# Kernel optimization log

Measured on AMD Instinct MI355X. Metric: run time of the kernel, lower is better.

The kernel has to match this reference:

```python
import jax, jax.numpy as jnp
import numpy as np

TEMPERATURE = 0.1
TOP_K = 8


def setup_inputs() -> dict:
    key = jax.random.key(0)
    k1, k2, k3 = jax.random.split(key, 3)
    num_tokens, d_model, num_experts = 32768, 2048, 64
    x = jax.random.normal(k1, (num_tokens, d_model), dtype=jnp.float32)
    # nn.Linear default init: U(-1/sqrt(fan_in), 1/sqrt(fan_in))
    bound = 1.0 / np.sqrt(d_model)
    W = jax.random.uniform(k2, (num_experts, d_model), jnp.float32, -bound, bound)
    b = jax.random.uniform(k3, (num_experts,), jnp.float32, -bound, bound)
    return {"x": x, "W": W, "b": b}


def reference(x, W, b):
    # gate: [T, E] = x @ W^T + b, scaled by temperature
    routing_logits = (jnp.einsum('td,ed->te', x, W) + b) / TEMPERATURE
    routing_probs = jax.nn.softmax(routing_logits, axis=-1)
    top_k_probs, top_k_indices = jax.lax.top_k(routing_probs, TOP_K)
    top_k_probs_normalized = top_k_probs / jnp.sum(top_k_probs, axis=-1, keepdims=True)
    return routing_logits, top_k_probs_normalized, top_k_indices
```

## Files before the change

### kernel.cpp

```cpp
#include <hip/hip_runtime.h>
#include <cstdint>

#define T_TOKENS 32768
#define D_MODEL  2048
#define N_EXP    64
#define BM       64
#define BK       64
#define CHUNKS   (D_MODEL / BK)
#define LDK      (BK + 8)

typedef short bf16x8 __attribute__((ext_vector_type(8)));
typedef unsigned short u16x8 __attribute__((ext_vector_type(8)));
typedef float f32x4 __attribute__((ext_vector_type(4)));

__device__ __forceinline__ unsigned short f2bf(float f) {
    union { float f; unsigned int u; } c; c.f = f;
    unsigned int u = c.u;
    u += 0x7fffu + ((u >> 16) & 1u);
    return (unsigned short)(u >> 16);
}
__device__ __forceinline__ float bf2f(unsigned short h) {
    union { float f; unsigned int u; } c; c.u = ((unsigned int)h) << 16;
    return c.f;
}

__device__ __forceinline__ void split3(const float4& a, const float4& b,
                                       u16x8& h, u16x8& m, u16x8& l) {
    float f[8] = {a.x, a.y, a.z, a.w, b.x, b.y, b.z, b.w};
#pragma unroll
    for (int i = 0; i < 8; ++i) {
        unsigned short hh = f2bf(f[i]);
        float r1 = f[i] - bf2f(hh);
        unsigned short mm = f2bf(r1);
        float r2 = r1 - bf2f(mm);
        unsigned short ll = f2bf(r2);
        h[i] = hh; m[i] = mm; l[i] = ll;
    }
}

__global__ __launch_bounds__(256, 2) void router_gemm(
    const float* __restrict__ x, const float* __restrict__ W,
    const float* __restrict__ b, float* __restrict__ logits)
{
    __shared__ unsigned short Ah[BM * LDK], Amid[BM * LDK], Alo[BM * LDK];
    __shared__ unsigned short Bh[N_EXP * LDK], Bmid[N_EXP * LDK], Blo[N_EXP * LDK];

    const int tid = threadIdx.x;
    const int t0  = blockIdx.x * BM;
    const int kq  = tid & 7;
    const int rid = tid >> 3;

    const float* xg = x + (long)(t0 + rid) * D_MODEL + kq * 8;
    const float* wg = W + (long)rid * D_MODEL + kq * 8;

    const int lane = tid & 63;
    const int w    = tid >> 6;
    const int ln   = lane & 15;
    const int kq8  = (lane >> 4) * 8;
    const int aoff = (w * 16 + ln) * LDK;

    f32x4 accA[4], accB[4];
#pragma unroll
    for (int j = 0; j < 4; ++j) { accA[j] = (f32x4)(0.f); accB[j] = (f32x4)(0.f); }

    float4 xr[2][2], wr[2][2];
#pragma unroll
    for (int p = 0; p < 2; ++p) {
        xr[p][0] = *(const float4*)(xg + (long)p * 32 * D_MODEL);
        xr[p][1] = *(const float4*)(xg + (long)p * 32 * D_MODEL + 4);
        wr[p][0] = *(const float4*)(wg + (long)p * 32 * D_MODEL);
        wr[p][1] = *(const float4*)(wg + (long)p * 32 * D_MODEL + 4);
    }

    for (int c = 0; c < CHUNKS; ++c) {
#pragma unroll
        for (int p = 0; p < 2; ++p) {
            const int row = rid + p * 32;
            u16x8 h, m, l;
            split3(xr[p][0], xr[p][1], h, m, l);
            *(u16x8*)&Ah  [row * LDK + kq * 8] = h;
            *(u16x8*)&Amid[row * LDK + kq * 8] = m;
            *(u16x8*)&Alo [row * LDK + kq * 8] = l;
            split3(wr[p][0], wr[p][1], h, m, l);
            *(u16x8*)&Bh  [row * LDK + kq * 8] = h;
            *(u16x8*)&Bmid[row * LDK + kq * 8] = m;
            *(u16x8*)&Blo [row * LDK + kq * 8] = l;
        }
        if (c + 1 < CHUNKS) {
            const float* xn = xg + (c + 1) * BK;
            const float* wn = wg + (c + 1) * BK;
#pragma unroll
            for (int p = 0; p < 2; ++p) {
                xr[p][0] = *(const float4*)(xn + (long)p * 32 * D_MODEL);
                xr[p][1] = *(const float4*)(xn + (long)p * 32 * D_MODEL + 4);
                wr[p][0] = *(const float4*)(wn + (long)p * 32 * D_MODEL);
                wr[p][1] = *(const float4*)(wn + (long)p * 32 * D_MODEL + 4);
            }
        }
        __syncthreads();
#pragma unroll
        for (int ks = 0; ks < 2; ++ks) {
            const int ko = ks * 32 + kq8;
            bf16x8 ah = *(const bf16x8*)&Ah  [aoff + ko];
            bf16x8 am = *(const bf16x8*)&Amid[aoff + ko];
            bf16x8 al = *(const bf16x8*)&Alo [aoff + ko];
#pragma unroll
            for (int j = 0; j < 4; ++j) {
                const int boff = (j * 16 + ln) * LDK + ko;
                bf16x8 bh = *(const bf16x8*)&Bh  [boff];
                bf16x8 bm = *(const bf16x8*)&Bmid[boff];
                bf16x8 bl = *(const bf16x8*)&Blo [boff];
                accA[j] = __builtin_amdgcn_mfma_f32_16x16x32_bf16(ah, bh, accA[j], 0, 0, 0);
                accB[j] = __builtin_amdgcn_mfma_f32_16x16x32_bf16(am, bh, accB[j], 0, 0, 0);
                accB[j] = __builtin_amdgcn_mfma_f32_16x16x32_bf16(ah, bm, accB[j], 0, 0, 0);
                accB[j] = __builtin_amdgcn_mfma_f32_16x16x32_bf16(al, bh, accB[j], 0, 0, 0);
                accB[j] = __builtin_amdgcn_mfma_f32_16x16x32_bf16(am, bm, accB[j], 0, 0, 0);
                accB[j] = __builtin_amdgcn_mfma_f32_16x16x32_bf16(ah, bl, accB[j], 0, 0, 0);
            }
        }
        __syncthreads();
    }

    float bias[4];
#pragma unroll
    for (int j = 0; j < 4; ++j) bias[j] = b[j * 16 + ln];
    const int trow = w * 16 + ((lane >> 4) << 2);
#pragma unroll
    for (int j = 0; j < 4; ++j) {
#pragma unroll
        for (int r = 0; r < 4; ++r) {
            float v = (accA[j][r] + accB[j][r] + bias[j]) / 0.1f;
            logits[(long)(t0 + trow + r) * N_EXP + j * 16 + ln] = v;
        }
    }
}

__global__ __launch_bounds__(256) void router_topk(
    const float* __restrict__ logits, float* __restrict__ probs, float* __restrict__ idxs)
{
    const int tid  = threadIdx.x;
    const int t    = blockIdx.x * 32 + (tid >> 3);
    const int s    = tid & 7;
    const int lane = tid & 63;

    const float* row = logits + (long)t * 64 + s * 8;
    float4 v0 = *(const float4*)row;
    float4 v1 = *(const float4*)(row + 4);
    float v[8] = {v0.x, v0.y, v0.z, v0.w, v1.x, v1.y, v1.z, v1.w};

    float sel_v = 0.f; int sel_i = 0;
#pragma unroll
    for (int p = 0; p < 8; ++p) {
        float bm = v[0]; int bi = s * 8;
#pragma unroll
        for (int i = 1; i < 8; ++i) {
            bool g = v[i] > bm;
            bm = g ? v[i] : bm;
            bi = g ? s * 8 + i : bi;
        }
#pragma unroll
        for (int d = 1; d < 8; d <<= 1) {
            float om = __shfl_xor(bm, d);
            int   oi = __shfl_xor(bi, d);
            bool take = (om > bm) || (om == bm && oi < bi);
            bm = take ? om : bm;
            bi = take ? oi : bi;
        }
        if (s == p) { sel_v = bm; sel_i = bi; }
#pragma unroll
        for (int i = 0; i < 8; ++i)
            if (s * 8 + i == bi) v[i] = -__builtin_inff();
    }

    float mx = __shfl(sel_v, lane & ~7);
    float wgt = expf(sel_v - mx);
    float sum = wgt;
#pragma unroll
    for (int d = 1; d < 8; d <<= 1) sum += __shfl_xor(sum, d);

    probs[(long)t * 8 + s] = wgt / sum;
    idxs [(long)t * 8 + s] = (float)sel_i;
}

extern "C" void kernel_launch(void* const* d_in, const int* in_sizes, int n_in,
                              void* d_out, int out_size, void* d_ws, size_t ws_size,
                              hipStream_t stream) {
    const float* x = (const float*)d_in[0];
    const float* W = (const float*)d_in[1];
    const float* b = (const float*)d_in[2];
    float* out    = (float*)d_out;
    float* logits = out;
    float* probs  = out + (long)T_TOKENS * N_EXP;
    float* idxs   = probs + (long)T_TOKENS * 8;

    router_gemm<<<dim3(T_TOKENS / BM), dim3(256), 0, stream>>>(x, W, b, logits);
    router_topk<<<dim3(T_TOKENS / 32), dim3(256), 0, stream>>>(logits, probs, idxs);
}
```

Before: 385.6 us.

## Pre-split W once into MFMA-ordered bf16 triples and double-buffer the x tile

A new prep kernel splits W into hi/mid/lo bf16 parts once per call and stores them in MFMA fragment order in the workspace. Each GEMM block then reads its B fragments straight from global memory (L2-resident) instead of reconverting W in every block and staging it in LDS. The x tile is double-buffered in LDS with a two-stage register prefetch, and the two accumulators are merged into one. This removes the redundant per-block W conversion and halves LDS use, at the cost of an extra launch, global B loads inside the MFMA loop, and a different summation order.

```diff
diff --git a/kernel.cpp b/kernel.cpp
--- a/kernel.cpp
+++ b/kernel.cpp
@@ -38,99 +38,113 @@
     }
 }
 
+__global__ void router_prep(const float* __restrict__ W, unsigned short* __restrict__ Wpk) {
+    const int t = blockIdx.x * 256 + threadIdx.x;
+    const int lane = t & 63;
+    const int sj = t >> 6;
+    const int e  = (sj & 3) * 16 + (lane & 15);
+    const int k0 = (sj >> 2) * 32 + (lane >> 4) * 8;
+    const float* src = W + (size_t)e * D_MODEL + k0;
+    float4 f0 = *(const float4*)src;
+    float4 f1 = *(const float4*)(src + 4);
+    u16x8 h, m, l;
+    split3(f0, f1, h, m, l);
+    unsigned short* dst = Wpk + (size_t)sj * 1536 + lane * 8;
+    *(u16x8*)(dst)        = h;
+    *(u16x8*)(dst + 512)  = m;
+    *(u16x8*)(dst + 1024) = l;
+}
+
+#define LOADX(R, CH) do {                                                     \
+    _Pragma("unroll") for (int p_ = 0; p_ < 2; ++p_) {                        \
+        const float* s_ = xg + (size_t)p_ * 32 * D_MODEL + (CH) * BK;         \
+        R[p_][0] = *(const float4*)s_;                                        \
+        R[p_][1] = *(const float4*)(s_ + 4);                                  \
+    } } while (0)
+
+#define CONV(R, BUF) do {                                                     \
+    _Pragma("unroll") for (int p_ = 0; p_ < 2; ++p_) {                        \
+        u16x8 h_, m_, l_;                                                     \
+        split3(R[p_][0], R[p_][1], h_, m_, l_);                               \
+        const int o_ = (rid + p_ * 32) * LDK + kq * 8;                        \
+        *(u16x8*)&Asm[BUF][0][o_] = h_;                                       \
+        *(u16x8*)&Asm[BUF][1][o_] = m_;                                       \
+        *(u16x8*)&Asm[BUF][2][o_] = l_;                                       \
+    } } while (0)
+
+#define COMPUTE(CH, BUF) do {                                                 \
+    _Pragma("unroll") for (int ks_ = 0; ks_ < 2; ++ks_) {                     \
+        const int ko_ = ks_ * 32 + kq8;                                       \
+        bf16x8 ah_ = *(const bf16x8*)&Asm[BUF][0][aoff + ko_];                \
+        bf16x8 am_ = *(const bf16x8*)&Asm[BUF][1][aoff + ko_];                \
+        bf16x8 al_ = *(const bf16x8*)&Asm[BUF][2][aoff + ko_];                \
+        _Pragma("unroll") for (int j_ = 0; j_ < 4; ++j_) {                    \
+            const unsigned short* wq_ = wlane + (size_t)(((CH)*2 + ks_)*4 + j_) * 1536; \
+            bf16x8 bh_ = *(const bf16x8*)(wq_);                               \
+            bf16x8 bm_ = *(const bf16x8*)(wq_ + 512);                         \
+            bf16x8 bl_ = *(const bf16x8*)(wq_ + 1024);                        \
+            acc[j_] = __builtin_amdgcn_mfma_f32_16x16x32_bf16(ah_, bh_, acc[j_], 0, 0, 0); \
+            acc[j_] = __builtin_amdgcn_mfma_f32_16x16x32_bf16(am_, bh_, acc[j_], 0, 0, 0); \
+            acc[j_] = __builtin_amdgcn_mfma_f32_16x16x32_bf16(ah_, bm_, acc[j_], 0, 0, 0); \
+            acc[j_] = __builtin_amdgcn_mfma_f32_16x16x32_bf16(al_, bh_, acc[j_], 0, 0, 0); \
+            acc[j_] = __builtin_amdgcn_mfma_f32_16x16x32_bf16(am_, bm_, acc[j_], 0, 0, 0); \
+            acc[j_] = __builtin_amdgcn_mfma_f32_16x16x32_bf16(ah_, bl_, acc[j_], 0, 0, 0); \
+        }                                                                     \
+    } } while (0)
+
 __global__ __launch_bounds__(256, 2) void router_gemm(
-    const float* __restrict__ x, const float* __restrict__ W,
+    const float* __restrict__ x, const unsigned short* __restrict__ Wpk,
     const float* __restrict__ b, float* __restrict__ logits)
 {
-    __shared__ unsigned short Ah[BM * LDK], Amid[BM * LDK], Alo[BM * LDK];
-    __shared__ unsigned short Bh[N_EXP * LDK], Bmid[N_EXP * LDK], Blo[N_EXP * LDK];
+    __shared__ unsigned short Asm[2][3][BM * LDK];
 
     const int tid = threadIdx.x;
     const int t0  = blockIdx.x * BM;
     const int kq  = tid & 7;
     const int rid = tid >> 3;
 
-    const float* xg = x + (long)(t0 + rid) * D_MODEL + kq * 8;
-    const float* wg = W + (long)rid * D_MODEL + kq * 8;
+    const float* xg = x + (size_t)(t0 + rid) * D_MODEL + kq * 8;
 
     const int lane = tid & 63;
     const int w    = tid >> 6;
     const int ln   = lane & 15;
     const int kq8  = (lane >> 4) * 8;
     const int aoff = (w * 16 + ln) * LDK;
-
-    f32x4 accA[4], accB[4];
-#pragma unroll
-    for (int j = 0; j < 4; ++j) { accA[j] = (f32x4)(0.f); accB[j] = (f32x4)(0.f); }
-
-    float4 xr[2][2], wr[2][2];
-#pragma unroll
-    for (int p = 0; p < 2; ++p) {
-        xr[p][0] = *(const float4*)(xg + (long)p * 32 * D_MODEL);
-        xr[p][1] = *(const float4*)(xg + (long)p * 32 * D_MODEL + 4);
-        wr[p][0] = *(const float4*)(wg + (long)p * 32 * D_MODEL);
-        wr[p][1] = *(const float4*)(wg + (long)p * 32 * D_MODEL + 4);
-    }
-
-    for (int c = 0; c < CHUNKS; ++c) {
-#pragma unroll
-        for (int p = 0; p < 2; ++p) {
-            const int row = rid + p * 32;
-            u16x8 h, m, l;
-            split3(xr[p][0], xr[p][1], h, m, l);
-            *(u16x8*)&Ah  [row * LDK + kq * 8] = h;
-            *(u16x8*)&Amid[row * LDK + kq * 8] = m;
-            *(u16x8*)&Alo [row * LDK + kq * 8] = l;
-            split3(wr[p][0], wr[p][1], h, m, l);
-            *(u16x8*)&Bh  [row * LDK + kq * 8] = h;
-            *(u16x8*)&Bmid[row * LDK + kq * 8] = m;
-            *(u16x8*)&Blo [row * LDK + kq * 8] = l;
-        }
-        if (c + 1 < CHUNKS) {
-            const float* xn = xg + (c + 1) * BK;
-            const float* wn = wg + (c + 1) * BK;
-#pragma unroll
-            for (int p = 0; p < 2; ++p) {
-                xr[p][0] = *(const float4*)(xn + (long)p * 32 * D_MODEL);
-                xr[p][1] = *(const float4*)(xn + (long)p * 32 * D_MODEL + 4);
-                wr[p][0] = *(const float4*)(wn + (long)p * 32 * D_MODEL);
-                wr[p][1] = *(const float4*)(wn + (long)p * 32 * D_MODEL + 4);
-            }
-        }
+    const unsigned short* wlane = Wpk + lane * 8;
+
+    f32x4 acc[4];
+#pragma unroll
+    for (int j = 0; j < 4; ++j) acc[j] = (f32x4)(0.f);
+
+    float4 ra[2][2], rb[2][2];
+
+    LOADX(ra, 0);
+    CONV(ra, 0);
+    LOADX(rb, 1);
+    __syncthreads();
+
+    for (int cc = 0; cc < CHUNKS; cc += 2) {
+        if (cc + 2 < CHUNKS) LOADX(ra, cc + 2);
+        CONV(rb, 1);
+        COMPUTE(cc, 0);
         __syncthreads();
-#pragma unroll
-        for (int ks = 0; ks < 2; ++ks) {
-            const int ko = ks * 32 + kq8;
-            bf16x8 ah = *(const bf16x8*)&Ah  [aoff + ko];
-            bf16x8 am = *(const bf16x8*)&Amid[aoff + ko];
-            bf16x8 al = *(const bf16x8*)&Alo [aoff + ko];
-#pragma unroll
-            for (int j = 0; j < 4; ++j) {
-                const int boff = (j * 16 + ln) * LDK + ko;
-                bf16x8 bh = *(const bf16x8*)&Bh  [boff];
-                bf16x8 bm = *(const bf16x8*)&Bmid[boff];
-                bf16x8 bl = *(const bf16x8*)&Blo [boff];
-                accA[j] = __builtin_amdgcn_mfma_f32_16x16x32_bf16(ah, bh, accA[j], 0, 0, 0);
-                accB[j] = __builtin_amdgcn_mfma_f32_16x16x32_bf16(am, bh, accB[j], 0, 0, 0);
-                accB[j] = __builtin_amdgcn_mfma_f32_16x16x32_bf16(ah, bm, accB[j], 0, 0, 0);
-                accB[j] = __builtin_amdgcn_mfma_f32_16x16x32_bf16(al, bh, accB[j], 0, 0, 0);
-                accB[j] = __builtin_amdgcn_mfma_f32_16x16x32_bf16(am, bm, accB[j], 0, 0, 0);
-                accB[j] = __builtin_amdgcn_mfma_f32_16x16x32_bf16(ah, bl, accB[j], 0, 0, 0);
-            }
-        }
+
+        if (cc + 3 < CHUNKS) LOADX(rb, cc + 3);
+        if (cc + 2 < CHUNKS) CONV(ra, 0);
+        COMPUTE(cc + 1, 1);
         __syncthreads();
     }
 
     float bias[4];
 #pragma unroll
     for (int j = 0; j < 4; ++j) bias[j] = b[j * 16 + ln];
-    const int trow = w * 16 + ((lane >> 4) << 2);
+    const int trow = w * 16 + (lane >> 4) * 4;
 #pragma unroll
     for (int j = 0; j < 4; ++j) {
 #pragma unroll
         for (int r = 0; r < 4; ++r) {
-            float v = (accA[j][r] + accB[j][r] + bias[j]) / 0.1f;
-            logits[(long)(t0 + trow + r) * N_EXP + j * 16 + ln] = v;
+            float v = (acc[j][r] + bias[j]) / 0.1f;
+            logits[(size_t)(t0 + trow + r) * N_EXP + j * 16 + ln] = v;
         }
     }
 }
@@ -143,7 +157,7 @@
     const int s    = tid & 7;
     const int lane = tid & 63;
 
-    const float* row = logits + (long)t * 64 + s * 8;
+    const float* row = logits + (size_t)t * 64 + s * 8;
     float4 v0 = *(const float4*)row;
     float4 v1 = *(const float4*)(row + 4);
     float v[8] = {v0.x, v0.y, v0.z, v0.w, v1.x, v1.y, v1.z, v1.w};
@@ -178,8 +192,8 @@
 #pragma unroll
     for (int d = 1; d < 8; d <<= 1) sum += __shfl_xor(sum, d);
 
-    probs[(long)t * 8 + s] = wgt / sum;
-    idxs [(long)t * 8 + s] = (float)sel_i;
+    probs[(size_t)t * 8 + s] = wgt / sum;
+    idxs [(size_t)t * 8 + s] = (float)sel_i;
 }
 
 extern "C" void kernel_launch(void* const* d_in, const int* in_sizes, int n_in,
@@ -190,9 +204,11 @@
     const float* b = (const float*)d_in[2];
     float* out    = (float*)d_out;
     float* logits = out;
-    float* probs  = out + (long)T_TOKENS * N_EXP;
-    float* idxs   = probs + (long)T_TOKENS * 8;
-
-    router_gemm<<<dim3(T_TOKENS / BM), dim3(256), 0, stream>>>(x, W, b, logits);
+    float* probs  = out + (size_t)T_TOKENS * N_EXP;
+    float* idxs   = probs + (size_t)T_TOKENS * 8;
+    unsigned short* Wpk = (unsigned short*)d_ws;
+
+    router_prep<<<dim3(64),            dim3(256), 0, stream>>>(W, Wpk);
+    router_gemm<<<dim3(T_TOKENS / BM), dim3(256), 0, stream>>>(x, Wpk, b, logits);
     router_topk<<<dim3(T_TOKENS / 32), dim3(256), 0, stream>>>(logits, probs, idxs);
 }
```

New measurement: 428.0 us. +11.0%, slower.
